# Kernel optimization log

Measured on AMD Instinct MI355X. Metric: run time of the kernel, lower is better.

## Reference

```python
import jax, jax.numpy as jnp
import numpy as np

DIM = 768
HEADS = 12
HEAD_DIM = DIM // HEADS


def setup_inputs() -> dict:
    key = jax.random.key(0)
    ks = jax.random.split(key, 5)
    B, S = 4, 2048
    init = 0.02
    x = jax.random.normal(ks[0], (B, S, DIM), dtype=jnp.float32)
    w_qkv = jax.random.normal(ks[1], (DIM, 3 * DIM), dtype=jnp.float32) * init
    b_qkv = jnp.zeros((3 * DIM,), dtype=jnp.float32)
    w_out = jax.random.normal(ks[2], (DIM, DIM), dtype=jnp.float32) * init
    b_out = jnp.zeros((DIM,), dtype=jnp.float32)
    return {"x": x, "w_qkv": w_qkv, "b_qkv": b_qkv, "w_out": w_out, "b_out": b_out}


def reference(x, w_qkv, b_qkv, w_out, b_out):
    B, S, D = x.shape
    # QKV projection: [B,S,3D] -> [3,B,H,S,hd]
    qkv = x @ w_qkv + b_qkv
    qkv = qkv.reshape(B, S, 3, HEADS, HEAD_DIM).transpose(2, 0, 3, 1, 4)
    q, k, v = qkv[0], qkv[1], qkv[2]
    # NOTE: original scales by 1/sqrt(head_num), not 1/sqrt(head_dim)
    scale = 1.0 / jnp.sqrt(jnp.float32(HEADS))
    scores = jnp.einsum("bhqd,bhkd->bhqk", q, k) * scale
    attn = jax.nn.softmax(scores, axis=-1)
    out = jnp.einsum("bhqk,bhkd->bhqd", attn, v)
    out = out.transpose(0, 2, 1, 3).reshape(B, S, D)
    return out @ w_out + b_out
```

## Files before the change

### kernel.cpp

```cpp
#include <hip/hip_runtime.h>
#include <hip/hip_bf16.h>
#include <cstdint>
#include <cstddef>

#define HEADS 12
#define HD    64
#define NB    4
#define SEQ   2048
#define DIM   768
#define NQKV  2304

static constexpr float QSCALE = 0.2886751345948129f * 1.4426950408889634f;

typedef __attribute__((ext_vector_type(8))) short short8;
typedef __attribute__((ext_vector_type(4))) short short4v;
typedef __attribute__((ext_vector_type(4))) float f32x4;

__device__ inline unsigned short f2bf(float x) {
    union { float f; uint32_t u; } v; v.f = x;
    return (unsigned short)((v.u + 0x7fffu + ((v.u >> 16) & 1u)) >> 16);
}

__device__ inline unsigned short f2bf_fast(float x) {
    __hip_bfloat16 h = __float2bfloat16(x);
    unsigned short u;
    __builtin_memcpy(&u, &h, 2);
    return u;
}

__device__ inline void gld16(const void* g, void* l) {
    __builtin_amdgcn_global_load_lds(
        (const __attribute__((address_space(1))) unsigned int*)g,
        (__attribute__((address_space(3))) unsigned int*)l, 16, 0, 0);
}

__global__ __launch_bounds__(256) void convert_x_kernel(
    const float* __restrict__ x, unsigned short* __restrict__ xb)
{
    const size_t i = ((size_t)blockIdx.x * 256 + threadIdx.x) * 8;
    const float4 a = *reinterpret_cast<const float4*>(x + i);
    const float4 b = *reinterpret_cast<const float4*>(x + i + 4);
    short8 o;
    o[0] = (short)f2bf(a.x); o[1] = (short)f2bf(a.y);
    o[2] = (short)f2bf(a.z); o[3] = (short)f2bf(a.w);
    o[4] = (short)f2bf(b.x); o[5] = (short)f2bf(b.y);
    o[6] = (short)f2bf(b.z); o[7] = (short)f2bf(b.w);
    *reinterpret_cast<short8*>(xb + i) = o;
}

__global__ __launch_bounds__(256) void transpose_w_kernel(
    const float* __restrict__ w, unsigned short* __restrict__ wT,
    int ncols , int nrows )
{
    __shared__ float tile[64][65];
    const int k0 = blockIdx.y * 64;
    const int n0 = blockIdx.x * 64;
    const int tr = threadIdx.x >> 4;
    const int tc4 = (threadIdx.x & 15) * 4;
    #pragma unroll
    for (int it = 0; it < 4; ++it) {
        const int kk = tr + it * 16;
        *reinterpret_cast<float4*>(&tile[kk][tc4]) =
            *reinterpret_cast<const float4*>(w + (size_t)(k0 + kk) * ncols + n0 + tc4);
    }
    __syncthreads();
    #pragma unroll
    for (int it = 0; it < 4; ++it) {
        const int nn = tr + it * 16;
        short4v o;
        #pragma unroll
        for (int r = 0; r < 4; ++r) o[r] = (short)f2bf(tile[tc4 + r][nn]);
        *reinterpret_cast<short4v*>(wT + (size_t)(n0 + nn) * nrows + k0 + tc4) = o;
    }
}

__global__ __launch_bounds__(256) void qkv_gemm_bf16(
    const unsigned short* __restrict__ A,
    const unsigned short* __restrict__ BT,
    const float* __restrict__ bias,
    unsigned short* __restrict__ qb, unsigned short* __restrict__ kb,
    unsigned short* __restrict__ vt)
{
    __shared__ __align__(16) unsigned short As[128][64];
    __shared__ __align__(16) unsigned short Bs[128][64];

    const int tid = threadIdx.x;
    const int wave = tid >> 6;
    const int lane = tid & 63;
    const int col = lane & 15;
    const int g = lane >> 4;
    const int m0 = blockIdx.y * 128;
    const int n0 = blockIdx.x * 128;
    const int wr = wave >> 1, wc = wave & 1;

    const int srow = tid >> 3;
    const int scl  = tid & 7;

    f32x4 acc[4][4] = {};

    for (int kt = 0; kt < DIM; kt += 64) {
        __syncthreads();
        #pragma unroll
        for (int it = 0; it < 4; ++it) {
            const int row = srow + it * 32;
            const int cg = scl ^ (row & 7);
            gld16(A + (size_t)(m0 + row) * DIM + kt + cg * 8,
                  &As[0][0] + (size_t)(it * 256 + wave * 64) * 8);
            gld16(BT + (size_t)(n0 + row) * DIM + kt + cg * 8,
                  &Bs[0][0] + (size_t)(it * 256 + wave * 64) * 8);
        }
        __syncthreads();

        #pragma unroll
        for (int ks = 0; ks < 2; ++ks) {
            short8 af[4], bf[4];
            #pragma unroll
            for (int i = 0; i < 4; ++i) {
                const int ra = wr * 64 + i * 16 + col;
                af[i] = *reinterpret_cast<const short8*>(
                    &As[ra][(((ks * 4 + g) ^ (ra & 7)) << 3)]);
                const int rb = wc * 64 + i * 16 + col;
                bf[i] = *reinterpret_cast<const short8*>(
                    &Bs[rb][(((ks * 4 + g) ^ (rb & 7)) << 3)]);
            }
            #pragma unroll
            for (int i = 0; i < 4; ++i)
                #pragma unroll
                for (int j = 0; j < 4; ++j)
                    acc[i][j] = __builtin_amdgcn_mfma_f32_16x16x32_bf16(
                        af[i], bf[j], acc[i][j], 0, 0, 0);
        }
    }

    const int which = n0 / DIM;
    #pragma unroll
    for (int j = 0; j < 4; ++j) {
        const int n = n0 + wc * 64 + j * 16 + col;
        const int rem = n - which * DIM;
        const int h = rem >> 6, dh = rem & 63;
        const float bj = bias[n];
        #pragma unroll
        for (int i = 0; i < 4; ++i) {
            const int mbase = m0 + wr * 64 + i * 16 + g * 4;
            const int b_ = mbase >> 11;
            const int s_ = mbase & 2047;
            const size_t bh = (size_t)(b_ * HEADS + h);
            if (which == 2) {
                short4v pk;
                #pragma unroll
                for (int r = 0; r < 4; ++r)
                    pk[r] = (short)f2bf(acc[i][j][r] + bj);
                *reinterpret_cast<short4v*>(vt + (bh * HD + dh) * SEQ + s_) = pk;
            } else {
                unsigned short* dst = (which == 0) ? qb : kb;
                const float sc = (which == 0) ? QSCALE : 1.0f;
                #pragma unroll
                for (int r = 0; r < 4; ++r)
                    dst[(bh * SEQ + s_ + r) * HD + dh] =
                        f2bf((acc[i][j][r] + bj) * sc);
            }
        }
    }
}

__global__ __launch_bounds__(256) void attn_kernel(
    const unsigned short* __restrict__ qb, const unsigned short* __restrict__ kbuf,
    const unsigned short* __restrict__ vt, unsigned short* __restrict__ ctxb)
{
    __shared__ __align__(16) unsigned short Ks[64][64];
    __shared__ __align__(16) unsigned short Vs[64][64];
    __shared__ __align__(16) unsigned short Ps[4][16][64];

    const int tid = threadIdx.x;
    const int wave = tid >> 6;
    const int lane = tid & 63;
    const int col = lane & 15;
    const int g   = lane >> 4;
    const int bh = blockIdx.y;
    const int q0 = blockIdx.x * 64;
    const int wq = q0 + wave * 16 + col;

    const size_t hb = (size_t)bh * SEQ * HD;

    short8 qf[2];
    {
        const unsigned short* src = qb + hb + (size_t)wq * HD + g * 8;
        qf[0] = *reinterpret_cast<const short8*>(src);
        qf[1] = *reinterpret_cast<const short8*>(src + 32);
    }

    f32x4 acc4[4] = {};
    float l_part = 0.0f;

    const unsigned short* Kg = kbuf + hb;
    const unsigned short* Vg = vt + hb;

    const int srow = tid >> 3;
    const int sc_  = tid & 7;

    for (int jt = 0; jt < SEQ / 64; ++jt) {
        const int kb0 = jt * 64;
        __syncthreads();
        #pragma unroll
        for (int it = 0; it < 2; ++it) {
            const int row = srow + it * 32;
            const int cg = sc_ ^ (row & 7);
            gld16(Kg + (size_t)(kb0 + row) * HD + cg * 8,
                  &Ks[0][0] + (size_t)(it * 256 + wave * 64) * 8);
            gld16(Vg + (size_t)row * SEQ + kb0 + cg * 8,
                  &Vs[0][0] + (size_t)(it * 256 + wave * 64) * 8);
        }
        __syncthreads();

        f32x4 st[4] = {};
        #pragma unroll
        for (int m = 0; m < 4; ++m) {
            const int row = m * 16 + col;
            const short8 kf0 = *reinterpret_cast<const short8*>(
                &Ks[row][((g ^ (row & 7)) << 3)]);
            const short8 kf1 = *reinterpret_cast<const short8*>(
                &Ks[row][(((g + 4) ^ (row & 7)) << 3)]);
            st[m] = __builtin_amdgcn_mfma_f32_16x16x32_bf16(kf0, qf[0], st[m], 0, 0, 0);
            st[m] = __builtin_amdgcn_mfma_f32_16x16x32_bf16(kf1, qf[1], st[m], 0, 0, 0);
        }

        float s0 = 0.0f, s1 = 0.0f, s2 = 0.0f, s3 = 0.0f;
        #pragma unroll
        for (int m = 0; m < 4; ++m) {
            float p[4];
            p[0] = __builtin_amdgcn_exp2f(st[m][0]);
            p[1] = __builtin_amdgcn_exp2f(st[m][1]);
            p[2] = __builtin_amdgcn_exp2f(st[m][2]);
            p[3] = __builtin_amdgcn_exp2f(st[m][3]);
            s0 += p[0]; s1 += p[1]; s2 += p[2]; s3 += p[3];
            short4v pk;
            #pragma unroll
            for (int r = 0; r < 4; ++r) pk[r] = (short)f2bf_fast(p[r]);
            const int scw = (2 * m + (g >> 1)) ^ (col & 7);
            *reinterpret_cast<short4v*>(
                &Ps[wave][col][(scw << 3) + ((g & 1) << 2)]) = pk;
        }
        l_part += (s0 + s1) + (s2 + s3);

        const short8 pf0 = *reinterpret_cast<const short8*>(
            &Ps[wave][col][((g ^ (col & 7)) << 3)]);
        const short8 pf1 = *reinterpret_cast<const short8*>(
            &Ps[wave][col][(((g + 4) ^ (col & 7)) << 3)]);

        #pragma unroll
        for (int nb = 0; nb < 4; ++nb) {
            const int row = nb * 16 + col;
            const short8 vf0 = *reinterpret_cast<const short8*>(
                &Vs[row][((g ^ (row & 7)) << 3)]);
            const short8 vf1 = *reinterpret_cast<const short8*>(
                &Vs[row][(((g + 4) ^ (row & 7)) << 3)]);
            acc4[nb] = __builtin_amdgcn_mfma_f32_16x16x32_bf16(pf0, vf0, acc4[nb], 0, 0, 0);
            acc4[nb] = __builtin_amdgcn_mfma_f32_16x16x32_bf16(pf1, vf1, acc4[nb], 0, 0, 0);
        }
    }

    float lt = l_part + __shfl_xor(l_part, 16);
    lt += __shfl_xor(lt, 32);
    float lr[4];
    #pragma unroll
    for (int r = 0; r < 4; ++r) lr[r] = 1.0f / __shfl(lt, g * 4 + r);
    const int b_ = bh / HEADS;
    const int h = bh - b_ * HEADS;
    #pragma unroll
    for (int nb = 0; nb < 4; ++nb)
        #pragma unroll
        for (int r = 0; r < 4; ++r) {
            const int s_ = q0 + wave * 16 + g * 4 + r;
            ctxb[((size_t)b_ * SEQ + s_) * DIM + h * HD + nb * 16 + col] =
                f2bf_fast(acc4[nb][r] * lr[r]);
        }
}

__global__ __launch_bounds__(256) void out_gemm_bf16(
    const unsigned short* __restrict__ A,
    const unsigned short* __restrict__ BT,
    const float* __restrict__ bias, float* __restrict__ out)
{
    __shared__ __align__(16) unsigned short As[128][64];
    __shared__ __align__(16) unsigned short Bs[128][64];

    const int tid = threadIdx.x;
    const int wave = tid >> 6;
    const int lane = tid & 63;
    const int col = lane & 15;
    const int g = lane >> 4;
    const int m0 = blockIdx.y * 128;
    const int n0 = blockIdx.x * 128;
    const int wr = wave >> 1, wc = wave & 1;

    const int srow = tid >> 3;
    const int scl  = tid & 7;

    f32x4 acc[4][4] = {};

    for (int kt = 0; kt < DIM; kt += 64) {
        __syncthreads();
        #pragma unroll
        for (int it = 0; it < 4; ++it) {
            const int row = srow + it * 32;
            const int cg = scl ^ (row & 7);
            gld16(A + (size_t)(m0 + row) * DIM + kt + cg * 8,
                  &As[0][0] + (size_t)(it * 256 + wave * 64) * 8);
            gld16(BT + (size_t)(n0 + row) * DIM + kt + cg * 8,
                  &Bs[0][0] + (size_t)(it * 256 + wave * 64) * 8);
        }
        __syncthreads();

        #pragma unroll
        for (int ks = 0; ks < 2; ++ks) {
            short8 af[4], bf[4];
            #pragma unroll
            for (int i = 0; i < 4; ++i) {
                const int ra = wr * 64 + i * 16 + col;
                af[i] = *reinterpret_cast<const short8*>(
                    &As[ra][(((ks * 4 + g) ^ (ra & 7)) << 3)]);
                const int rb = wc * 64 + i * 16 + col;
                bf[i] = *reinterpret_cast<const short8*>(
                    &Bs[rb][(((ks * 4 + g) ^ (rb & 7)) << 3)]);
            }
            #pragma unroll
            for (int i = 0; i < 4; ++i)
                #pragma unroll
                for (int j = 0; j < 4; ++j)
                    acc[i][j] = __builtin_amdgcn_mfma_f32_16x16x32_bf16(
                        af[i], bf[j], acc[i][j], 0, 0, 0);
        }
    }

    #pragma unroll
    for (int j = 0; j < 4; ++j) {
        const int n = n0 + wc * 64 + j * 16 + col;
        const float bj = bias[n];
        #pragma unroll
        for (int i = 0; i < 4; ++i) {
            const int m = m0 + wr * 64 + i * 16 + g * 4;
            #pragma unroll
            for (int r = 0; r < 4; ++r)
                out[(size_t)(m + r) * DIM + n] = acc[i][j][r] + bj;
        }
    }
}

extern "C" void kernel_launch(void* const* d_in, const int* in_sizes, int n_in,
                              void* d_out, int out_size, void* d_ws, size_t ws_size,
                              hipStream_t stream)
{
    const float* x     = (const float*)d_in[0];
    const float* w_qkv = (const float*)d_in[1];
    const float* b_qkv = (const float*)d_in[2];
    const float* w_out = (const float*)d_in[3];
    const float* b_out = (const float*)d_in[4];
    float* out = (float*)d_out;

    const size_t QSZ = (size_t)NB * HEADS * SEQ * HD;
    unsigned short* qb   = (unsigned short*)d_ws;
    unsigned short* kb   = qb + QSZ;
    unsigned short* vt   = kb + QSZ;
    unsigned short* xb   = vt + QSZ;
    unsigned short* ctxb = xb + QSZ;
    unsigned short* wqT  = ctxb + QSZ;
    unsigned short* woT  = wqT + (size_t)NQKV * DIM;

    convert_x_kernel<<<3072, 256, 0, stream>>>(x, xb);
    transpose_w_kernel<<<dim3(NQKV / 64, DIM / 64), 256, 0, stream>>>(
        w_qkv, wqT, NQKV, DIM);
    transpose_w_kernel<<<dim3(DIM / 64, DIM / 64), 256, 0, stream>>>(
        w_out, woT, DIM, DIM);

    qkv_gemm_bf16<<<dim3(NQKV / 128, (NB * SEQ) / 128), 256, 0, stream>>>(
        xb, wqT, b_qkv, qb, kb, vt);
    attn_kernel<<<dim3(SEQ / 64, NB * HEADS), 256, 0, stream>>>(qb, kb, vt, ctxb);
    out_gemm_bf16<<<dim3(DIM / 128, (NB * SEQ) / 128), 256, 0, stream>>>(
        ctxb, woT, b_out, out);
}
```

Before: 172.2 us.

## Double-buffer K/V tiles in attention kernel with async prefetch and MFMA priority

The attention kernel now keeps two shared-memory buffers for K and V tiles and issues the direct-to-LDS global loads for the next tile before computing on the current one, so load latency overlaps with the MFMA and softmax work. Explicit vmcnt waits and raw s_barrier calls replace the paired __syncthreads. s_setprio raises wave priority around the MFMA sections. In exchange, LDS use doubles, which may lower occupancy, and correctness depends on the hand-counted vmcnt value.

```diff
diff --git a/kernel.cpp b/kernel.cpp
--- a/kernel.cpp
+++ b/kernel.cpp
@@ -167,8 +167,8 @@
     const unsigned short* __restrict__ qb, const unsigned short* __restrict__ kbuf,
     const unsigned short* __restrict__ vt, unsigned short* __restrict__ ctxb)
 {
-    __shared__ __align__(16) unsigned short Ks[64][64];
-    __shared__ __align__(16) unsigned short Vs[64][64];
+    __shared__ __align__(16) unsigned short Ks[2][64][64];
+    __shared__ __align__(16) unsigned short Vs[2][64][64];
     __shared__ __align__(16) unsigned short Ps[4][16][64];
 
     const int tid = threadIdx.x;
@@ -198,31 +198,45 @@
     const int srow = tid >> 3;
     const int sc_  = tid & 7;
 
-    for (int jt = 0; jt < SEQ / 64; ++jt) {
+    auto STAGE = [&](int jt, int bsel) {
         const int kb0 = jt * 64;
-        __syncthreads();
         #pragma unroll
         for (int it = 0; it < 2; ++it) {
             const int row = srow + it * 32;
             const int cg = sc_ ^ (row & 7);
             gld16(Kg + (size_t)(kb0 + row) * HD + cg * 8,
-                  &Ks[0][0] + (size_t)(it * 256 + wave * 64) * 8);
+                  &Ks[bsel][0][0] + (size_t)(it * 256 + wave * 64) * 8);
             gld16(Vg + (size_t)row * SEQ + kb0 + cg * 8,
-                  &Vs[0][0] + (size_t)(it * 256 + wave * 64) * 8);
-        }
-        __syncthreads();
+                  &Vs[bsel][0][0] + (size_t)(it * 256 + wave * 64) * 8);
+        }
+    };
+
+    const int NT = SEQ / 64;
+    STAGE(0, 0);
+
+    for (int jt = 0; jt < NT; ++jt) {
+        const int cur = jt & 1;
+        if (jt + 1 < NT) {
+            STAGE(jt + 1, cur ^ 1);
+            asm volatile("s_waitcnt vmcnt(4)" ::: "memory");
+        } else {
+            asm volatile("s_waitcnt vmcnt(0)" ::: "memory");
+        }
+        __builtin_amdgcn_s_barrier();
 
         f32x4 st[4] = {};
+        __builtin_amdgcn_s_setprio(1);
         #pragma unroll
         for (int m = 0; m < 4; ++m) {
             const int row = m * 16 + col;
             const short8 kf0 = *reinterpret_cast<const short8*>(
-                &Ks[row][((g ^ (row & 7)) << 3)]);
+                &Ks[cur][row][((g ^ (row & 7)) << 3)]);
             const short8 kf1 = *reinterpret_cast<const short8*>(
-                &Ks[row][(((g + 4) ^ (row & 7)) << 3)]);
+                &Ks[cur][row][(((g + 4) ^ (row & 7)) << 3)]);
             st[m] = __builtin_amdgcn_mfma_f32_16x16x32_bf16(kf0, qf[0], st[m], 0, 0, 0);
             st[m] = __builtin_amdgcn_mfma_f32_16x16x32_bf16(kf1, qf[1], st[m], 0, 0, 0);
         }
+        __builtin_amdgcn_s_setprio(0);
 
         float s0 = 0.0f, s1 = 0.0f, s2 = 0.0f, s3 = 0.0f;
         #pragma unroll
@@ -247,16 +261,20 @@
         const short8 pf1 = *reinterpret_cast<const short8*>(
             &Ps[wave][col][(((g + 4) ^ (col & 7)) << 3)]);
 
+        __builtin_amdgcn_s_setprio(1);
         #pragma unroll
         for (int nb = 0; nb < 4; ++nb) {
             const int row = nb * 16 + col;
             const short8 vf0 = *reinterpret_cast<const short8*>(
-                &Vs[row][((g ^ (row & 7)) << 3)]);
+                &Vs[cur][row][((g ^ (row & 7)) << 3)]);
             const short8 vf1 = *reinterpret_cast<const short8*>(
-                &Vs[row][(((g + 4) ^ (row & 7)) << 3)]);
+                &Vs[cur][row][(((g + 4) ^ (row & 7)) << 3)]);
             acc4[nb] = __builtin_amdgcn_mfma_f32_16x16x32_bf16(pf0, vf0, acc4[nb], 0, 0, 0);
             acc4[nb] = __builtin_amdgcn_mfma_f32_16x16x32_bf16(pf1, vf1, acc4[nb], 0, 0, 0);
         }
+        __builtin_amdgcn_s_setprio(0);
+
+        __builtin_amdgcn_s_barrier();
     }
 
     float lt = l_part + __shfl_xor(l_part, 16);
```

Result: no change. 173.8 us (+0.9%).

## Load K/V fragments directly from global into registers, drop LDS staging and barriers

Applied to the files above, without the earlier changes.

The attention kernel no longer stages K and V tiles through shared memory with two block barriers per key tile. Each wave now loads its own K and V MFMA fragments straight from global memory into registers, relying on L1/L2 for reuse across the four waves, and wraps the MFMA sections in s_setprio. This removes the barrier stalls and the LDS traffic, but each block now issues four times the global/L2 loads and the loads sit exposed without explicit prefetching.

```diff
diff --git a/kernel.cpp b/kernel.cpp
--- a/kernel.cpp
+++ b/kernel.cpp
@@ -167,8 +167,6 @@
     const unsigned short* __restrict__ qb, const unsigned short* __restrict__ kbuf,
     const unsigned short* __restrict__ vt, unsigned short* __restrict__ ctxb)
 {
-    __shared__ __align__(16) unsigned short Ks[64][64];
-    __shared__ __align__(16) unsigned short Vs[64][64];
     __shared__ __align__(16) unsigned short Ps[4][16][64];
 
     const int tid = threadIdx.x;
@@ -192,36 +190,35 @@
     f32x4 acc4[4] = {};
     float l_part = 0.0f;
 
-    const unsigned short* Kg = kbuf + hb;
-    const unsigned short* Vg = vt + hb;
-
-    const int srow = tid >> 3;
-    const int sc_  = tid & 7;
+    const unsigned short* Kp = kbuf + hb + (size_t)col * HD + g * 8;
+    const unsigned short* Vp = vt + hb + (size_t)col * SEQ + g * 8;
 
     for (int jt = 0; jt < SEQ / 64; ++jt) {
         const int kb0 = jt * 64;
-        __syncthreads();
-        #pragma unroll
-        for (int it = 0; it < 2; ++it) {
-            const int row = srow + it * 32;
-            const int cg = sc_ ^ (row & 7);
-            gld16(Kg + (size_t)(kb0 + row) * HD + cg * 8,
-                  &Ks[0][0] + (size_t)(it * 256 + wave * 64) * 8);
-            gld16(Vg + (size_t)row * SEQ + kb0 + cg * 8,
-                  &Vs[0][0] + (size_t)(it * 256 + wave * 64) * 8);
-        }
-        __syncthreads();
+
+        short8 kf[4][2];
+        #pragma unroll
+        for (int m = 0; m < 4; ++m) {
+            const unsigned short* src = Kp + (size_t)(kb0 + m * 16) * HD;
+            kf[m][0] = *reinterpret_cast<const short8*>(src);
+            kf[m][1] = *reinterpret_cast<const short8*>(src + 32);
+        }
 
         f32x4 st[4] = {};
+        __builtin_amdgcn_s_setprio(1);
         #pragma unroll
         for (int m = 0; m < 4; ++m) {
-            const int row = m * 16 + col;
-            const short8 kf0 = *reinterpret_cast<const short8*>(
-                &Ks[row][((g ^ (row & 7)) << 3)]);
-            const short8 kf1 = *reinterpret_cast<const short8*>(
-                &Ks[row][(((g + 4) ^ (row & 7)) << 3)]);
-            st[m] = __builtin_amdgcn_mfma_f32_16x16x32_bf16(kf0, qf[0], st[m], 0, 0, 0);
-            st[m] = __builtin_amdgcn_mfma_f32_16x16x32_bf16(kf1, qf[1], st[m], 0, 0, 0);
+            st[m] = __builtin_amdgcn_mfma_f32_16x16x32_bf16(kf[m][0], qf[0], st[m], 0, 0, 0);
+            st[m] = __builtin_amdgcn_mfma_f32_16x16x32_bf16(kf[m][1], qf[1], st[m], 0, 0, 0);
+        }
+        __builtin_amdgcn_s_setprio(0);
+
+        short8 vf[4][2];
+        #pragma unroll
+        for (int nb = 0; nb < 4; ++nb) {
+            const unsigned short* src = Vp + (size_t)(nb * 16) * SEQ + kb0;
+            vf[nb][0] = *reinterpret_cast<const short8*>(src);
+            vf[nb][1] = *reinterpret_cast<const short8*>(src + 32);
         }
 
         float s0 = 0.0f, s1 = 0.0f, s2 = 0.0f, s3 = 0.0f;
@@ -247,16 +244,13 @@
         const short8 pf1 = *reinterpret_cast<const short8*>(
             &Ps[wave][col][(((g + 4) ^ (col & 7)) << 3)]);
 
+        __builtin_amdgcn_s_setprio(1);
         #pragma unroll
         for (int nb = 0; nb < 4; ++nb) {
-            const int row = nb * 16 + col;
-            const short8 vf0 = *reinterpret_cast<const short8*>(
-                &Vs[row][((g ^ (row & 7)) << 3)]);
-            const short8 vf1 = *reinterpret_cast<const short8*>(
-                &Vs[row][(((g + 4) ^ (row & 7)) << 3)]);
-            acc4[nb] = __builtin_amdgcn_mfma_f32_16x16x32_bf16(pf0, vf0, acc4[nb], 0, 0, 0);
-            acc4[nb] = __builtin_amdgcn_mfma_f32_16x16x32_bf16(pf1, vf1, acc4[nb], 0, 0, 0);
-        }
+            acc4[nb] = __builtin_amdgcn_mfma_f32_16x16x32_bf16(pf0, vf[nb][0], acc4[nb], 0, 0, 0);
+            acc4[nb] = __builtin_amdgcn_mfma_f32_16x16x32_bf16(pf1, vf[nb][1], acc4[nb], 0, 0, 0);
+        }
+        __builtin_amdgcn_s_setprio(0);
     }
 
     float lt = l_part + __shfl_xor(l_part, 16);
```

After: 426.1 us. 147% more time.
